# Optimization experiments

Hardware: AMD Instinct MI355X
Metric: run time of the kernel (lower is better)

The kernel has to match this reference:

```python
import jax, jax.numpy as jnp
import numpy as np

EMBED = 1024
HEADS = 16
HEAD_DIM = EMBED // HEADS


def _rope(t):
    # t: (B, S, H, D) -> rotary embedding applied over last dim (GPT-NeoX rotate-half)
    B, S, H, D = t.shape
    half = D // 2
    inv_freq = 1.0 / (10000.0 ** (jnp.arange(0, half, dtype=jnp.float32) / half))
    freqs = jnp.arange(S, dtype=jnp.float32)[:, None] * inv_freq[None, :]  # (S, half)
    cos = jnp.cos(freqs)[None, :, None, :]
    sin = jnp.sin(freqs)[None, :, None, :]
    t1, t2 = t[..., :half], t[..., half:]
    return jnp.concatenate([t1 * cos - t2 * sin, t2 * cos + t1 * sin], axis=-1)


def setup_inputs() -> dict:
    key = jax.random.key(0)
    k1, k2, k3 = jax.random.split(key, 3)
    B, S = 2, 2048
    x = jax.random.normal(k1, (B, S, EMBED), dtype=jnp.float32)
    attn_mask = jnp.ones((B, S), dtype=bool)
    w_qkv = jax.random.normal(k2, (EMBED, 3 * EMBED), dtype=jnp.float32) * (1.0 / np.sqrt(EMBED))
    w_out = jax.random.normal(k3, (EMBED, EMBED), dtype=jnp.float32) * (1.0 / np.sqrt(EMBED))
    return {"x": x, "attn_mask": attn_mask, "w_qkv": w_qkv, "w_out": w_out, "is_causal": 1}


def reference(x, attn_mask, w_qkv, w_out, is_causal):
    B, S, E = x.shape
    qkv = x @ w_qkv                                   # (B, S, 3E)
    q, k, v = jnp.split(qkv, 3, axis=-1)
    q = q.reshape(B, S, HEADS, HEAD_DIM)
    k = k.reshape(B, S, HEADS, HEAD_DIM)
    v = v.reshape(B, S, HEADS, HEAD_DIM)
    q = _rope(q)
    k = _rope(k)
    scale = 1.0 / np.sqrt(HEAD_DIM)
    scores = jnp.einsum('bqhd,bkhd->bhqk', q, k) * scale  # (B, H, S, S)
    neg = jnp.asarray(-1e30, dtype=scores.dtype)
    if is_causal:
        causal = jnp.tril(jnp.ones((S, S), dtype=bool))
        scores = jnp.where(causal[None, None], scores, neg)
    else:
        scores = jnp.where(attn_mask[:, None, None, :], scores, neg)
    attn = jax.nn.softmax(scores, axis=-1)
    y = jnp.einsum('bhqk,bkhd->bqhd', attn, v).reshape(B, S, E)
    return y @ w_out
```

## Files before the change

### kernel.cpp

```cpp
#include <hip/hip_runtime.h>
#include <hip/hip_bf16.h>
#include <stdint.h>

typedef float v4f __attribute__((ext_vector_type(4)));
typedef short v8s __attribute__((ext_vector_type(8)));

#define LOG2E 1.44269504088896f
#define QSCALE (0.125f * LOG2E)
#define SOFTMAX_OFF 16.0f

__device__ __forceinline__ unsigned short f2bf(float f) {
    unsigned int u = __float_as_uint(f);
    u += 0x7fffu + ((u >> 16) & 1u);
    return (unsigned short)(u >> 16);
}

#define LDS_FENCE() __builtin_amdgcn_fence(__ATOMIC_ACQ_REL, "workgroup")

__device__ __forceinline__ void gload_lds16(const unsigned short* g, unsigned short* s) {
    __builtin_amdgcn_global_load_lds(
        (const __attribute__((address_space(1))) unsigned int*)g,
        (__attribute__((address_space(3))) unsigned int*)s, 16, 0, 0);
}

#define PIPE_BARRIER_KEEP4()                                   \
    do {                                                       \
        asm volatile("s_waitcnt vmcnt(4)" ::: "memory");       \
        __builtin_amdgcn_s_barrier();                          \
        asm volatile("" ::: "memory");                         \
    } while (0)
#define PIPE_BARRIER_DRAIN()                                   \
    do {                                                       \
        asm volatile("s_waitcnt vmcnt(0)" ::: "memory");       \
        __builtin_amdgcn_s_barrier();                          \
        asm volatile("" ::: "memory");                         \
    } while (0)

__global__ void k_prep(const float* __restrict__ x,
                       const float* __restrict__ w_qkv,
                       const float* __restrict__ w_out,
                       unsigned short* __restrict__ xb,
                       unsigned short* __restrict__ wqkvT,
                       unsigned short* __restrict__ woutT,
                       float2* __restrict__ rope) {
    __shared__ unsigned short tile[64][65];
    int id = blockIdx.x, t = threadIdx.x;
    if (id < 1024) {
        int base = id * 256 + t;
#pragma unroll
        for (int k = 0; k < 4; ++k) {
            int i = base + k * 262144;
            float4 v = ((const float4*)x)[i];
            ushort4 o;
            o.x = f2bf(v.x); o.y = f2bf(v.y); o.z = f2bf(v.z); o.w = f2bf(v.w);
            ((ushort4*)xb)[i] = o;
        }
        return;
    }
    id -= 1024;
    if (id < 256) {
        int idx = id * 256 + t;
        int s = idx >> 5, d = idx & 31;
        float inv = __expf(-(float)d * 0.28782313662425572f);
        float sn, cs;
        sincosf((float)s * inv, &sn, &cs);
        rope[idx] = make_float2(cs, sn);
        return;
    }
    id -= 256;
    const float* src; unsigned short* dst; int N, kb, nb;
    if (id < 768) { src = w_qkv; dst = wqkvT; N = 3072; nb = (id % 48) * 64; kb = (id / 48) * 64; }
    else { id -= 768; src = w_out; dst = woutT; N = 1024; nb = (id % 16) * 64; kb = (id / 16) * 64; }
    const int K = 1024;
    for (int i = 0; i < 16; ++i) {
        int e = t + i * 256;
        int n_l = e & 63, k_l = e >> 6;
        tile[n_l][k_l] = f2bf(src[(size_t)(kb + k_l) * N + nb + n_l]);
    }
    __syncthreads();
    for (int i = 0; i < 16; ++i) {
        int e = t + i * 256;
        int k_l = e & 63, n_l = e >> 6;
        dst[(size_t)(nb + n_l) * K + kb + k_l] = tile[n_l][k_l];
    }
}

__global__ __launch_bounds__(256) void k_gemm_qkv(
    const unsigned short* __restrict__ A,
    const unsigned short* __restrict__ Bt,
    const float2* __restrict__ rope,
    unsigned short* __restrict__ Qg,
    unsigned short* __restrict__ Kg,
    unsigned short* __restrict__ Vt) {
    const int K = 1024;
    __shared__ __align__(16) union {
        struct { unsigned short Ab[3][4096], Bb[3][4096]; } g;
        unsigned short vt[2][64][136];
    } sm;
    const int t = threadIdx.x;
    const int w = t >> 6, l = t & 63, quad = l >> 4, ln = l & 15;
    const int wm = (w >> 1) * 64, wn = (w & 1) * 64;
    const int mb = blockIdx.y * 128, nb = blockIdx.x * 128;

    v4f acc[4][4];
#pragma unroll
    for (int i = 0; i < 4; ++i)
#pragma unroll
        for (int j = 0; j < 4; ++j) acc[i][j] = (v4f){0.f, 0.f, 0.f, 0.f};

    auto stage = [&](int buf, int k0) {
#pragma unroll
        for (int u = 0; u < 2; ++u) {
            int e = t + u * 256;
            gload_lds16(A + (size_t)(mb + (e >> 2)) * K + k0 + (e & 3) * 8,
                        &sm.g.Ab[buf][(w * 64 + u * 256) * 8]);
            gload_lds16(Bt + (size_t)(nb + (e >> 2)) * K + k0 + (e & 3) * 8,
                        &sm.g.Bb[buf][(w * 64 + u * 256) * 8]);
        }
    };

    stage(0, 0);
    stage(1, 32);
    int cur = 0, nxt = 2;
    for (int itk = 0; itk < 32; ++itk) {
        if (itk < 31) PIPE_BARRIER_KEEP4();
        else          PIPE_BARRIER_DRAIN();
        if (itk + 2 < 32) {
            stage(nxt, (itk + 2) * 32);
            nxt = nxt == 2 ? 0 : nxt + 1;
        }
        v8s af[4], bfr[4];
#pragma unroll
        for (int i = 0; i < 4; ++i)
            af[i] = *(const v8s*)&sm.g.Ab[cur][(wm + i * 16 + ln) * 32 + quad * 8];
#pragma unroll
        for (int j = 0; j < 4; ++j)
            bfr[j] = *(const v8s*)&sm.g.Bb[cur][(wn + j * 16 + ln) * 32 + quad * 8];
#pragma unroll
        for (int i = 0; i < 4; ++i)
#pragma unroll
            for (int j = 0; j < 4; ++j)
                acc[i][j] = __builtin_amdgcn_mfma_f32_16x16x32_bf16(
                    af[i], bfr[j], acc[i][j], 0, 0, 0);
        cur = cur == 2 ? 0 : cur + 1;
    }

    if (nb >= 2048) {
        __syncthreads();
        const int hh = wn >> 6;
#pragma unroll
        for (int i = 0; i < 4; ++i)
#pragma unroll
            for (int j = 0; j < 4; ++j) {
                int d = j * 16 + ln;
#pragma unroll
                for (int r = 0; r < 4; ++r)
                    sm.vt[hh][d][wm + i * 16 + quad * 4 + r] = f2bf(acc[i][j][r]);
            }
        __syncthreads();
        const int hbase = (nb & 1023) >> 6;
        const int b = mb >> 11, sbase = mb & 2047;
#pragma unroll
        for (int i = 0; i < 8; ++i) {
            int c = t + i * 256;
            int h2 = c >> 10, dd = (c >> 4) & 63, off = (c & 15) * 8;
            v8s val = *(const v8s*)&sm.vt[h2][dd][off];
            *(v8s*)(Vt + ((size_t)((b * 16 + hbase + h2) * 64 + dd) * 2048 + sbase + off)) = val;
        }
        return;
    }

    const int region = (nb + wn) >> 10;
    const int h = ((nb + wn) & 1023) >> 6;
    unsigned short* dst = region == 0 ? Qg : Kg;
    const float scale = region == 0 ? QSCALE : 1.0f;
#pragma unroll
    for (int jj = 0; jj < 2; ++jj) {
        const float2* rp = rope + jj * 16 + ln;
#pragma unroll
        for (int i = 0; i < 4; ++i)
#pragma unroll
            for (int r = 0; r < 4; ++r) {
                int row = mb + wm + i * 16 + quad * 4 + r;
                int s = row & 2047, b = row >> 11;
                float2 cs = rp[s * 32];
                float t1 = acc[i][jj][r], t2 = acc[i][jj + 2][r];
                size_t base = ((size_t)(b * 16 + h) * 2048 + s) * 64;
                dst[base + jj * 16 + ln]      = f2bf((t1 * cs.x - t2 * cs.y) * scale);
                dst[base + jj * 16 + ln + 32] = f2bf((t2 * cs.x + t1 * cs.y) * scale);
            }
    }
}

__global__ __launch_bounds__(256) void k_gemm_out(
    const unsigned short* __restrict__ A,
    const unsigned short* __restrict__ Bt,
    float* __restrict__ C) {
    const int K = 1024, N = 1024;
    __shared__ __align__(16) unsigned short Ab[3][4096];
    __shared__ __align__(16) unsigned short Bb[3][4096];
    const int t = threadIdx.x;
    const int w = t >> 6, l = t & 63, quad = l >> 4, ln = l & 15;
    const int wm = (w >> 1) * 64, wn = (w & 1) * 64;
    const int mb = blockIdx.y * 128, nb = blockIdx.x * 128;

    v4f acc[4][4];
#pragma unroll
    for (int i = 0; i < 4; ++i)
#pragma unroll
        for (int j = 0; j < 4; ++j) acc[i][j] = (v4f){0.f, 0.f, 0.f, 0.f};

    auto stage = [&](int buf, int k0) {
#pragma unroll
        for (int u = 0; u < 2; ++u) {
            int e = t + u * 256;
            gload_lds16(A + (size_t)(mb + (e >> 2)) * K + k0 + (e & 3) * 8,
                        &Ab[buf][(w * 64 + u * 256) * 8]);
            gload_lds16(Bt + (size_t)(nb + (e >> 2)) * K + k0 + (e & 3) * 8,
                        &Bb[buf][(w * 64 + u * 256) * 8]);
        }
    };

    stage(0, 0);
    stage(1, 32);
    int cur = 0, nxt = 2;
    for (int itk = 0; itk < 32; ++itk) {
        if (itk < 31) PIPE_BARRIER_KEEP4();
        else          PIPE_BARRIER_DRAIN();
        if (itk + 2 < 32) {
            stage(nxt, (itk + 2) * 32);
            nxt = nxt == 2 ? 0 : nxt + 1;
        }
        v8s af[4], bfr[4];
#pragma unroll
        for (int i = 0; i < 4; ++i)
            af[i] = *(const v8s*)&Ab[cur][(wm + i * 16 + ln) * 32 + quad * 8];
#pragma unroll
        for (int j = 0; j < 4; ++j)
            bfr[j] = *(const v8s*)&Bb[cur][(wn + j * 16 + ln) * 32 + quad * 8];
#pragma unroll
        for (int i = 0; i < 4; ++i)
#pragma unroll
            for (int j = 0; j < 4; ++j)
                acc[i][j] = __builtin_amdgcn_mfma_f32_16x16x32_bf16(
                    af[i], bfr[j], acc[i][j], 0, 0, 0);
        cur = cur == 2 ? 0 : cur + 1;
    }

#pragma unroll
    for (int i = 0; i < 4; ++i) {
        int r0 = mb + wm + i * 16 + quad * 4;
#pragma unroll
        for (int j = 0; j < 4; ++j) {
            int c0 = nb + wn + j * 16 + ln;
#pragma unroll
            for (int r = 0; r < 4; ++r)
                C[(size_t)(r0 + r) * N + c0] = acc[i][j][r];
        }
    }
}

__global__ __launch_bounds__(256) void k_flash(
    const unsigned short* __restrict__ Qg,
    const unsigned short* __restrict__ Kg,
    const unsigned short* __restrict__ Vt,
    unsigned short* __restrict__ Og) {
    __shared__ __align__(16) unsigned short Kb[2][64 * 64];
    __shared__ __align__(16) unsigned short Vb[2][64 * 64];
    __shared__ __align__(16) unsigned short P[4][16][72];

    const int id = blockIdx.x;
    const int xcd = id & 7, slot = id >> 3;
    const int bh = xcd * 4 + (slot & 3);
    const int qt = 31 - (slot >> 2);
    const int qbase = qt * 64;
    const int nit = qt + 1;

    const int t = threadIdx.x, w = t >> 6, l = t & 63, quad = l >> 4, ln = l & 15;
    const int b = bh >> 4, h = bh & 15;

    const unsigned short* Qp = Qg + (size_t)bh * 2048 * 64;
    const unsigned short* Kp = Kg + (size_t)bh * 2048 * 64;
    const unsigned short* Vp = Vt + (size_t)bh * 64 * 2048;

    unsigned kst[2], vst[2];
    int cchunk = l & 7, rloc = l >> 3;
#pragma unroll
    for (int j = 0; j < 2; ++j) {
        int c = w + j * 4;
        int rr = c * 8 + rloc;
        int g = (cchunk + rr) & 7;
        kst[j] = (unsigned)(rr * 64 + g * 8);
        vst[j] = (unsigned)(rr * 2048 + g * 8);
    }
    const int c0 = ((quad - ln) & 7) * 8;
    const int c1 = ((quad + 4 - ln) & 7) * 8;
    const v8s ones = {0x3F80, 0x3F80, 0x3F80, 0x3F80, 0x3F80, 0x3F80, 0x3F80, 0x3F80};

    const int qrow = qbase + w * 16 + ln;
    v8s qf0 = *(const v8s*)(Qp + (size_t)qrow * 64 + quad * 8);
    v8s qf1 = *(const v8s*)(Qp + (size_t)qrow * 64 + quad * 8 + 32);

    v4f oacc[5];
#pragma unroll
    for (int dt = 0; dt < 5; ++dt) oacc[dt] = (v4f){0.f, 0.f, 0.f, 0.f};

    auto stage = [&](int buf, int kvb) {
        const unsigned short* kg = Kp + (size_t)kvb * 64;
        const unsigned short* vg = Vp + kvb;
#pragma unroll
        for (int j = 0; j < 2; ++j) {
            int c = w + j * 4;
            gload_lds16(kg + kst[j], &Kb[buf][c * 512]);
            gload_lds16(vg + vst[j], &Vb[buf][c * 512]);
        }
    };

    auto compute = [&](int buf, int it) {
        v4f sc[4];
#pragma unroll
        for (int kt = 0; kt < 4; ++kt) {
            int row = kt * 16 + ln;
            v8s k0 = *(const v8s*)&Kb[buf][row * 64 + c0];
            v8s k1 = *(const v8s*)&Kb[buf][row * 64 + c1];
            sc[kt] = (v4f){0.f, 0.f, 0.f, 0.f};
            sc[kt] = __builtin_amdgcn_mfma_f32_16x16x32_bf16(qf0, k0, sc[kt], 0, 0, 0);
            sc[kt] = __builtin_amdgcn_mfma_f32_16x16x32_bf16(qf1, k1, sc[kt], 0, 0, 0);
        }
        if (it == qt) {
            int q0 = qbase + w * 16 + quad * 4;
#pragma unroll
            for (int kt = 0; kt < 4; ++kt) {
                int kv = qbase + kt * 16 + ln;
#pragma unroll
                for (int r = 0; r < 4; ++r)
                    if (kv > q0 + r) sc[kt][r] = -1e30f;
            }
        }
#pragma unroll
        for (int kt = 0; kt < 4; ++kt)
#pragma unroll
            for (int r = 0; r < 4; ++r)
                sc[kt][r] = exp2f(sc[kt][r] - SOFTMAX_OFF);

#pragma unroll
        for (int kt = 0; kt < 4; ++kt) {
            union { __hip_bfloat162 hh; unsigned int u; } p01, p23;
            p01.hh = __float22bfloat162_rn(make_float2(sc[kt][0], sc[kt][1]));
            p23.hh = __float22bfloat162_rn(make_float2(sc[kt][2], sc[kt][3]));
            P[w][quad * 4 + 0][kt * 16 + ln] = (unsigned short)p01.u;
            P[w][quad * 4 + 1][kt * 16 + ln] = (unsigned short)(p01.u >> 16);
            P[w][quad * 4 + 2][kt * 16 + ln] = (unsigned short)p23.u;
            P[w][quad * 4 + 3][kt * 16 + ln] = (unsigned short)(p23.u >> 16);
        }
        LDS_FENCE();
        v8s pf0 = *(const v8s*)&P[w][ln][quad * 8];
        v8s pf1 = *(const v8s*)&P[w][ln][quad * 8 + 32];
        LDS_FENCE();
#pragma unroll
        for (int dt = 0; dt < 4; ++dt) {
            int row = dt * 16 + ln;
            v8s v0 = *(const v8s*)&Vb[buf][row * 64 + c0];
            v8s v1 = *(const v8s*)&Vb[buf][row * 64 + c1];
            oacc[dt] = __builtin_amdgcn_mfma_f32_16x16x32_bf16(pf0, v0, oacc[dt], 0, 0, 0);
            oacc[dt] = __builtin_amdgcn_mfma_f32_16x16x32_bf16(pf1, v1, oacc[dt], 0, 0, 0);
        }
        oacc[4] = __builtin_amdgcn_mfma_f32_16x16x32_bf16(pf0, ones, oacc[4], 0, 0, 0);
        oacc[4] = __builtin_amdgcn_mfma_f32_16x16x32_bf16(pf1, ones, oacc[4], 0, 0, 0);
    };

    stage(0, 0);
    int it = 0;
    for (;;) {
        __syncthreads();
        stage(1, (it + 1) * 64);
        compute(0, it);
        if (++it >= nit) break;
        __syncthreads();
        stage(0, (it + 1) * 64);
        compute(1, it);
        if (++it >= nit) break;
    }

    float rden[4];
#pragma unroll
    for (int r = 0; r < 4; ++r) rden[r] = 1.f / oacc[4][r];
#pragma unroll
    for (int dt = 0; dt < 4; ++dt)
#pragma unroll
        for (int r = 0; r < 4; ++r) {
            int s = qbase + w * 16 + quad * 4 + r;
            Og[(size_t)(b * 2048 + s) * 1024 + h * 64 + dt * 16 + ln] =
                f2bf(oacc[dt][r] * rden[r]);
        }
}

extern "C" void kernel_launch(void* const* d_in, const int* in_sizes, int n_in,
                              void* d_out, int out_size, void* d_ws, size_t ws_size,
                              hipStream_t stream) {
    const float* x     = (const float*)d_in[0];
    const float* w_qkv = (const float*)d_in[2];
    const float* w_out = (const float*)d_in[3];
    char* ws = (char*)d_ws;

    unsigned short* xb    = (unsigned short*)(ws);
    unsigned short* wqkvT = (unsigned short*)(ws + (size_t)(8 << 20));
    unsigned short* woutT = (unsigned short*)(ws + (size_t)(14 << 20));
    unsigned short* Qg    = (unsigned short*)(ws + (size_t)(16 << 20));
    unsigned short* Kg    = (unsigned short*)(ws + (size_t)(24 << 20));
    unsigned short* Vt    = (unsigned short*)(ws + (size_t)(32 << 20));
    unsigned short* Og    = (unsigned short*)(ws + (size_t)(40 << 20));
    float2*         rope  = (float2*)(ws + (size_t)(48 << 20));

    k_prep<<<2304, 256, 0, stream>>>(x, w_qkv, w_out, xb, wqkvT, woutT, rope);
    k_gemm_qkv<<<dim3(24, 32), 256, 0, stream>>>(xb, wqkvT, rope, Qg, Kg, Vt);
    k_flash<<<1024, 256, 0, stream>>>(Qg, Kg, Vt, Og);
    k_gemm_out<<<dim3(8, 32), 256, 0, stream>>>(Og, woutT, (float*)d_out);
}
```

Measured before the change: 193.3 us.

## Enlarge QKV GEMM tile to 256x256 with 8 waves, swizzled LDS and interleaved staging

Rewrites the QKV projection GEMM to use 256x256 output tiles with 512 threads and a K step of 64. Fragment loads go through an XOR-swizzled LDS layout to avoid bank conflicts. Loads for the next tile are split into four chunks and interleaved between MFMA phases, with s_setprio raised around each MFMA burst. The aim is more data reuse per LDS byte and better overlap of memory and compute. The trade-off is a grid of only 192 blocks, which leaves some CUs idle, plus much higher LDS and register use per block; the V-transpose epilogue is widened to match.

```diff
diff --git a/kernel.cpp b/kernel.cpp
--- a/kernel.cpp
+++ b/kernel.cpp
@@ -22,6 +22,9 @@
         (const __attribute__((address_space(1))) unsigned int*)g,
         (__attribute__((address_space(3))) unsigned int*)s, 16, 0, 0);
 }
+
+#define BAR()      asm volatile("s_barrier" ::: "memory")
+#define VMWAIT(N)  asm volatile("s_waitcnt vmcnt(" #N ")" ::: "memory")
 
 #define PIPE_BARRIER_KEEP4()                                   \
     do {                                                       \
@@ -85,7 +88,7 @@
     }
 }
 
-__global__ __launch_bounds__(256) void k_gemm_qkv(
+__global__ __launch_bounds__(512, 2) void k_gemm_qkv(
     const unsigned short* __restrict__ A,
     const unsigned short* __restrict__ Bt,
     const float2* __restrict__ rope,
@@ -94,94 +97,135 @@
     unsigned short* __restrict__ Vt) {
     const int K = 1024;
     __shared__ __align__(16) union {
-        struct { unsigned short Ab[3][4096], Bb[3][4096]; } g;
-        unsigned short vt[2][64][136];
+        struct { unsigned short Ab[2][256 * 64], Bb[2][256 * 64]; } g;
+        unsigned short vt[4][64][264];
     } sm;
     const int t = threadIdx.x;
     const int w = t >> 6, l = t & 63, quad = l >> 4, ln = l & 15;
-    const int wm = (w >> 1) * 64, wn = (w & 1) * 64;
-    const int mb = blockIdx.y * 128, nb = blockIdx.x * 128;
-
-    v4f acc[4][4];
-#pragma unroll
-    for (int i = 0; i < 4; ++i)
+    const int wr = w >> 2, wc = w & 3;
+    const int mb = blockIdx.y * 256, nb = blockIdx.x * 256;
+    const int lxr = l >> 3;
+    const int swz = ((l & 7) ^ lxr) * 8;
+
+    v4f acc[8][4];
+#pragma unroll
+    for (int i = 0; i < 8; ++i)
 #pragma unroll
         for (int j = 0; j < 4; ++j) acc[i][j] = (v4f){0.f, 0.f, 0.f, 0.f};
 
-    auto stage = [&](int buf, int k0) {
-#pragma unroll
-        for (int u = 0; u < 2; ++u) {
-            int e = t + u * 256;
-            gload_lds16(A + (size_t)(mb + (e >> 2)) * K + k0 + (e & 3) * 8,
-                        &sm.g.Ab[buf][(w * 64 + u * 256) * 8]);
-            gload_lds16(Bt + (size_t)(nb + (e >> 2)) * K + k0 + (e & 3) * 8,
-                        &sm.g.Bb[buf][(w * 64 + u * 256) * 8]);
+    auto stageHT = [&](const unsigned short* src, int grow, int k0, unsigned short* lds) {
+#pragma unroll
+        for (int c = 0; c < 2; ++c) {
+            int r0 = w * 16 + c * 8;
+            gload_lds16(src + (size_t)(grow + r0 + lxr) * K + k0 + swz, lds + r0 * 64);
         }
     };
-
-    stage(0, 0);
-    stage(1, 32);
-    int cur = 0, nxt = 2;
-    for (int itk = 0; itk < 32; ++itk) {
-        if (itk < 31) PIPE_BARRIER_KEEP4();
-        else          PIPE_BARRIER_DRAIN();
-        if (itk + 2 < 32) {
-            stage(nxt, (itk + 2) * 32);
-            nxt = nxt == 2 ? 0 : nxt + 1;
-        }
-        v8s af[4], bfr[4];
-#pragma unroll
-        for (int i = 0; i < 4; ++i)
-            af[i] = *(const v8s*)&sm.g.Ab[cur][(wm + i * 16 + ln) * 32 + quad * 8];
-#pragma unroll
-        for (int j = 0; j < 4; ++j)
-            bfr[j] = *(const v8s*)&sm.g.Bb[cur][(wn + j * 16 + ln) * 32 + quad * 8];
-#pragma unroll
-        for (int i = 0; i < 4; ++i)
-#pragma unroll
-            for (int j = 0; j < 4; ++j)
-                acc[i][j] = __builtin_amdgcn_mfma_f32_16x16x32_bf16(
-                    af[i], bfr[j], acc[i][j], 0, 0, 0);
-        cur = cur == 2 ? 0 : cur + 1;
+    auto frag = [&](const unsigned short* base, int row, int g16) -> v8s {
+        return *(const v8s*)&base[row * 64 + ((g16 ^ (row & 7)) << 3)];
+    };
+
+    stageHT(A,  mb,       0,  &sm.g.Ab[0][0]);
+    stageHT(A,  mb + 128, 0,  &sm.g.Ab[0][128 * 64]);
+    stageHT(Bt, nb,       0,  &sm.g.Bb[0][0]);
+    stageHT(Bt, nb + 128, 0,  &sm.g.Bb[0][128 * 64]);
+    stageHT(A,  mb,       64, &sm.g.Ab[1][0]);
+    stageHT(A,  mb + 128, 64, &sm.g.Ab[1][128 * 64]);
+    VMWAIT(4);
+    BAR();
+
+    for (int kt = 0; kt < 16; ++kt) {
+        const int buf = kt & 1, nbf = buf ^ 1;
+        const unsigned short* Ap = &sm.g.Ab[buf][0];
+        const unsigned short* Bp = &sm.g.Bb[buf][0];
+        if (kt + 1 < 16) stageHT(Bt, nb, (kt + 1) * 64, &sm.g.Bb[nbf][0]);
+        v8s a0[8], b0[4];
+#pragma unroll
+        for (int i = 0; i < 8; ++i) a0[i] = frag(Ap, wr * 128 + i * 16 + ln, quad);
+#pragma unroll
+        for (int j = 0; j < 4; ++j) b0[j] = frag(Bp, wc * 64 + j * 16 + ln, quad);
+        __builtin_amdgcn_s_setprio(1);
+#pragma unroll
+        for (int i = 0; i < 8; ++i) {
+            acc[i][0] = __builtin_amdgcn_mfma_f32_16x16x32_bf16(a0[i], b0[0], acc[i][0], 0, 0, 0);
+            acc[i][1] = __builtin_amdgcn_mfma_f32_16x16x32_bf16(a0[i], b0[1], acc[i][1], 0, 0, 0);
+        }
+        __builtin_amdgcn_s_setprio(0);
+        BAR();
+        if (kt + 1 < 16) stageHT(Bt, nb + 128, (kt + 1) * 64, &sm.g.Bb[nbf][128 * 64]);
+        v8s a1[8], b1[4];
+#pragma unroll
+        for (int i = 0; i < 8; ++i) a1[i] = frag(Ap, wr * 128 + i * 16 + ln, 4 + quad);
+#pragma unroll
+        for (int j = 0; j < 4; ++j) b1[j] = frag(Bp, wc * 64 + j * 16 + ln, 4 + quad);
+        __builtin_amdgcn_s_setprio(1);
+#pragma unroll
+        for (int i = 0; i < 8; ++i) {
+            acc[i][2] = __builtin_amdgcn_mfma_f32_16x16x32_bf16(a0[i], b0[2], acc[i][2], 0, 0, 0);
+            acc[i][3] = __builtin_amdgcn_mfma_f32_16x16x32_bf16(a0[i], b0[3], acc[i][3], 0, 0, 0);
+        }
+        __builtin_amdgcn_s_setprio(0);
+        BAR();
+        if (kt + 2 < 16) stageHT(A, mb, (kt + 2) * 64, &sm.g.Ab[buf][0]);
+        __builtin_amdgcn_s_setprio(1);
+#pragma unroll
+        for (int i = 0; i < 8; ++i) {
+            acc[i][0] = __builtin_amdgcn_mfma_f32_16x16x32_bf16(a1[i], b1[0], acc[i][0], 0, 0, 0);
+            acc[i][1] = __builtin_amdgcn_mfma_f32_16x16x32_bf16(a1[i], b1[1], acc[i][1], 0, 0, 0);
+        }
+        __builtin_amdgcn_s_setprio(0);
+        BAR();
+        if (kt + 2 < 16) stageHT(A, mb + 128, (kt + 2) * 64, &sm.g.Ab[buf][128 * 64]);
+        __builtin_amdgcn_s_setprio(1);
+#pragma unroll
+        for (int i = 0; i < 8; ++i) {
+            acc[i][2] = __builtin_amdgcn_mfma_f32_16x16x32_bf16(a1[i], b1[2], acc[i][2], 0, 0, 0);
+            acc[i][3] = __builtin_amdgcn_mfma_f32_16x16x32_bf16(a1[i], b1[3], acc[i][3], 0, 0, 0);
+        }
+        __builtin_amdgcn_s_setprio(0);
+        if (kt < 14)       VMWAIT(4);
+        else if (kt == 14) VMWAIT(0);
+        if (kt < 15) BAR();
     }
 
     if (nb >= 2048) {
         __syncthreads();
-        const int hh = wn >> 6;
-#pragma unroll
-        for (int i = 0; i < 4; ++i)
+#pragma unroll
+        for (int i = 0; i < 8; ++i)
 #pragma unroll
             for (int j = 0; j < 4; ++j) {
                 int d = j * 16 + ln;
-#pragma unroll
-                for (int r = 0; r < 4; ++r)
-                    sm.vt[hh][d][wm + i * 16 + quad * 4 + r] = f2bf(acc[i][j][r]);
+                int s0 = wr * 128 + i * 16 + quad * 4;
+                ushort4 pk;
+                pk.x = f2bf(acc[i][j][0]); pk.y = f2bf(acc[i][j][1]);
+                pk.z = f2bf(acc[i][j][2]); pk.w = f2bf(acc[i][j][3]);
+                *(ushort4*)&sm.vt[wc][d][s0] = pk;
             }
         __syncthreads();
         const int hbase = (nb & 1023) >> 6;
         const int b = mb >> 11, sbase = mb & 2047;
 #pragma unroll
-        for (int i = 0; i < 8; ++i) {
-            int c = t + i * 256;
-            int h2 = c >> 10, dd = (c >> 4) & 63, off = (c & 15) * 8;
+        for (int i = 0; i < 16; ++i) {
+            int c = t + i * 512;
+            int h2 = c >> 11, dd = (c >> 5) & 63, off = (c & 31) * 8;
             v8s val = *(const v8s*)&sm.vt[h2][dd][off];
             *(v8s*)(Vt + ((size_t)((b * 16 + hbase + h2) * 64 + dd) * 2048 + sbase + off)) = val;
         }
         return;
     }
 
-    const int region = (nb + wn) >> 10;
-    const int h = ((nb + wn) & 1023) >> 6;
+    const int nbw = nb + wc * 64;
+    const int region = nbw >> 10;
+    const int h = (nbw & 1023) >> 6;
     unsigned short* dst = region == 0 ? Qg : Kg;
     const float scale = region == 0 ? QSCALE : 1.0f;
 #pragma unroll
     for (int jj = 0; jj < 2; ++jj) {
         const float2* rp = rope + jj * 16 + ln;
 #pragma unroll
-        for (int i = 0; i < 4; ++i)
+        for (int i = 0; i < 8; ++i)
 #pragma unroll
             for (int r = 0; r < 4; ++r) {
-                int row = mb + wm + i * 16 + quad * 4 + r;
+                int row = mb + wr * 128 + i * 16 + quad * 4 + r;
                 int s = row & 2047, b = row >> 11;
                 float2 cs = rp[s * 32];
                 float t1 = acc[i][jj][r], t2 = acc[i][jj + 2][r];
@@ -413,7 +457,7 @@
     float2*         rope  = (float2*)(ws + (size_t)(48 << 20));
 
     k_prep<<<2304, 256, 0, stream>>>(x, w_qkv, w_out, xb, wqkvT, woutT, rope);
-    k_gemm_qkv<<<dim3(24, 32), 256, 0, stream>>>(xb, wqkvT, rope, Qg, Kg, Vt);
+    k_gemm_qkv<<<dim3(12, 16), 512, 0, stream>>>(xb, wqkvT, rope, Qg, Kg, Vt);
     k_flash<<<1024, 256, 0, stream>>>(Qg, Kg, Vt, Og);
     k_gemm_out<<<dim3(8, 32), 256, 0, stream>>>(Og, woutT, (float*)d_out);
 }
```

Measured after the change: 199.2 us. +3.1%, slower.
